# Kernel tuning notes

Measured on AMD Instinct MI355X. Metric: run time of the kernel, lower is better.

## Reference

```python
import jax, jax.numpy as jnp
import numpy as np

N_HEADS = 4


def setup_inputs() -> dict:
    key = jax.random.key(0)
    ks = jax.random.split(key, 6)
    B, T, N, D = 4, 16, 64, 256
    x = jax.random.normal(ks[0], (B, T, N, D), dtype=jnp.float32)
    bias_features = jax.random.normal(ks[1], (B, T, N, N, D), dtype=jnp.float32)
    mask = jax.random.randint(ks[2], (B, T, N), 0, 2).astype(bool)
    s = 1.0 / np.sqrt(D).astype(np.float32)
    Wqkv = jax.random.normal(ks[3], (D, 3 * D), dtype=jnp.float32) * s
    bqkv = jnp.zeros((3 * D,), dtype=jnp.float32)
    Wproj = jax.random.normal(ks[4], (D, D), dtype=jnp.float32) * s
    bproj = jnp.zeros((D,), dtype=jnp.float32)
    return {"x": x, "bias_features": bias_features, "mask": mask,
            "Wqkv": Wqkv, "bqkv": bqkv, "Wproj": Wproj, "bproj": bproj}


def reference(x, bias_features, mask, Wqkv, bqkv, Wproj, bproj):
    B, T, N, D = x.shape
    H = N_HEADS
    hd = D // H
    Batch = B * T
    scale = 1.0 / float(np.sqrt(hd))

    x_flat = x.reshape(Batch, N, D)
    qkv = x_flat @ Wqkv + bqkv                      # (Batch, N, 3D)
    q, k, v = jnp.split(qkv, 3, axis=-1)
    q = q.reshape(Batch, N, H, hd).transpose(0, 2, 1, 3)   # (Batch, H, N, hd)
    k = k.reshape(Batch, N, H, hd).transpose(0, 2, 1, 3)
    v = v.reshape(Batch, N, H, hd).transpose(0, 2, 1, 3)

    # geometry bias: (Batch, H, N, N, hd)
    b_geo = bias_features.reshape(Batch, N, N, H, hd).transpose(0, 3, 1, 2, 4)
    # per-pair dot of q[n] with geometry feature for pair (n, m)
    rel_scores = jnp.einsum("bhnd,bhnmd->bhnm", q, b_geo) * scale

    mask_flat = mask.reshape(Batch, 1, 1, N)
    attn_bias = jnp.where(mask_flat, rel_scores, jnp.float32(-1e9))

    scores = jnp.einsum("bhnd,bhmd->bhnm", q, k) * scale + attn_bias
    attn = jax.nn.softmax(scores, axis=-1)
    out = jnp.einsum("bhnm,bhmd->bhnd", attn, v)    # (Batch, H, N, hd)

    out = out.transpose(0, 2, 1, 3).reshape(Batch, N, D)
    out = out @ Wproj + bproj
    return out.reshape(B, T, N, D)
```

## Files before the change

kernel.cpp:

```cpp
#include <hip/hip_runtime.h>
#include <hip/hip_bf16.h>

#define BATCH 64
#define NRES 64
#define DMODEL 256
#define ROWS (BATCH*NRES)
#define QKVC 768
#define SCALE 0.125f
#define LDP 68

typedef float floatx4 __attribute__((ext_vector_type(4)));

__global__ __launch_bounds__(256) void qkv_gemm(
    const float* __restrict__ x, const float* __restrict__ W,
    const float* __restrict__ bq, float* __restrict__ qkv) {
  __shared__ float AsT[64 * LDP];
  __shared__ float Bs[64 * LDP];
  int t = threadIdx.x;
  int tx = t & 15, ty = t >> 4;
  int rowBase = blockIdx.y * 64;
  int colBase = blockIdx.x * 64;
  float acc[4][4] = {};
  for (int kb = 0; kb < 256; kb += 64) {
#pragma unroll
    for (int p = 0; p < 4; ++p) {
      int e = (p * 256 + t) * 4;
      int r = e >> 6, c = e & 63;
      float4 av = *(const float4*)&x[(size_t)(rowBase + r) * 256 + kb + c];
      AsT[(c + 0) * LDP + r] = av.x;
      AsT[(c + 1) * LDP + r] = av.y;
      AsT[(c + 2) * LDP + r] = av.z;
      AsT[(c + 3) * LDP + r] = av.w;
      *(float4*)&Bs[r * LDP + c] =
          *(const float4*)&W[(size_t)(kb + r) * QKVC + colBase + c];
    }
    __syncthreads();
#pragma unroll 4
    for (int kk = 0; kk < 64; ++kk) {
      float4 a4 = *(const float4*)&AsT[kk * LDP + ty * 4];
      float4 b4 = *(const float4*)&Bs[kk * LDP + tx * 4];
      float a[4] = {a4.x, a4.y, a4.z, a4.w};
      float b[4] = {b4.x, b4.y, b4.z, b4.w};
#pragma unroll
      for (int i = 0; i < 4; ++i)
#pragma unroll
        for (int j = 0; j < 4; ++j) acc[i][j] += a[i] * b[j];
    }
    __syncthreads();
  }
#pragma unroll
  for (int i = 0; i < 4; ++i) {
    int r = rowBase + ty * 4 + i;
#pragma unroll
    for (int j = 0; j < 4; ++j) {
      int c = colBase + tx * 4 + j;
      qkv[(size_t)r * QKVC + c] = acc[i][j] + bq[c];
    }
  }
}

__global__ __launch_bounds__(256) void qk_gemm(const float* __restrict__ qkv,
                                               float* __restrict__ qk) {
  __shared__ float qs[64 * 65];
  __shared__ float ks[64 * 65];
  int t = threadIdx.x;
  int bh = blockIdx.x;
  int b = bh >> 2, h = bh & 3;
  for (int i = 0; i < 16; ++i) {
    int idx = i * 256 + t;
    int r = idx >> 6, d = idx & 63;
    qs[r * 65 + d] = qkv[(size_t)(b * 64 + r) * QKVC + h * 64 + d];
    ks[r * 65 + d] = qkv[(size_t)(b * 64 + r) * QKVC + 256 + h * 64 + d];
  }
  __syncthreads();
  int m = t & 63, nq = t >> 6;
  for (int ni = 0; ni < 16; ++ni) {
    int n = nq * 16 + ni;
    float s = 0.f;
#pragma unroll 16
    for (int d = 0; d < 64; ++d) s += qs[n * 65 + d] * ks[m * 65 + d];
    qk[((size_t)bh * 64 + n) * 64 + m] = s;
  }
}

__global__ __launch_bounds__(256) void attn_kernel(
    const float* __restrict__ bias, const int* __restrict__ mask,
    const float* __restrict__ qkv, const float* __restrict__ qk,
    float* __restrict__ ctx) {
  __shared__ float q_s[256];
  __shared__ int mask_s[64];
  __shared__ float rel_s[256];
  __shared__ float attn_s[256];
  int t = threadIdx.x;
  int blk = blockIdx.x;
  int b = blk >> 6;
  int n_res = blk & 63;
  int m = t & 63, h = t >> 6;
  float s_qk = qk[(((size_t)(b * 4 + h) * 64 + n_res) * 64) + m];
  int msk = mask[b * 64 + m];
  if (t < 64) mask_s[t] = mask[b * 64 + t];
  q_s[t] = qkv[(size_t)blk * QKVC + t];
  __syncthreads();
  int wave = t >> 6, lane = t & 63;
  int hseg = lane >> 4;
  float4 qv = *(const float4*)&q_s[lane * 4];
  const floatx4* brow_base =
      (const floatx4*)(bias + (size_t)blk * 64 * 256);
#pragma unroll
  for (int i = 0; i < 16; ++i) {
    int mm = i * 4 + wave;
    if (mask_s[mm]) {
      floatx4 bv = __builtin_nontemporal_load(&brow_base[mm * 64 + lane]);
      float p = bv.x * qv.x + bv.y * qv.y + bv.z * qv.z + bv.w * qv.w;
      p += __shfl_xor(p, 1, 64);
      p += __shfl_xor(p, 2, 64);
      p += __shfl_xor(p, 4, 64);
      p += __shfl_xor(p, 8, 64);
      if ((lane & 15) == 0) rel_s[hseg * 64 + mm] = p;
    }
  }
  __syncthreads();
  float rel = rel_s[h * 64 + m];
  float logit = s_qk * SCALE + (msk ? rel * SCALE : -1e9f);
  float mx = logit;
#pragma unroll
  for (int off = 32; off > 0; off >>= 1) mx = fmaxf(mx, __shfl_xor(mx, off, 64));
  float ex = __expf(logit - mx);
  float sm = ex;
#pragma unroll
  for (int off = 32; off > 0; off >>= 1) sm += __shfl_xor(sm, off, 64);
  attn_s[h * 64 + m] = ex / sm;
  __syncthreads();
  int c = t;
  int hh = c >> 6;
  float acc = 0.f;
  const float* vbase = qkv + (size_t)b * 64 * QKVC + 512 + c;
#pragma unroll 8
  for (int mm = 0; mm < 64; ++mm) acc += attn_s[hh * 64 + mm] * vbase[(size_t)mm * QKVC];
  ctx[(size_t)blk * 256 + c] = acc;
}

__global__ __launch_bounds__(256) void proj_gemm(
    const float* __restrict__ ctx, const float* __restrict__ W,
    const float* __restrict__ bp, float* __restrict__ out) {
  __shared__ float AsT[64 * LDP];
  __shared__ float Bs[64 * LDP];
  int t = threadIdx.x;
  int tx = t & 15, ty = t >> 4;
  int rowBase = blockIdx.y * 64;
  int colBase = blockIdx.x * 64;
  float acc[4][4] = {};
  for (int kb = 0; kb < 256; kb += 64) {
#pragma unroll
    for (int p = 0; p < 4; ++p) {
      int e = (p * 256 + t) * 4;
      int r = e >> 6, c = e & 63;
      float4 av = *(const float4*)&ctx[(size_t)(rowBase + r) * 256 + kb + c];
      AsT[(c + 0) * LDP + r] = av.x;
      AsT[(c + 1) * LDP + r] = av.y;
      AsT[(c + 2) * LDP + r] = av.z;
      AsT[(c + 3) * LDP + r] = av.w;
      *(float4*)&Bs[r * LDP + c] =
          *(const float4*)&W[(size_t)(kb + r) * 256 + colBase + c];
    }
    __syncthreads();
#pragma unroll 4
    for (int kk = 0; kk < 64; ++kk) {
      float4 a4 = *(const float4*)&AsT[kk * LDP + ty * 4];
      float4 b4 = *(const float4*)&Bs[kk * LDP + tx * 4];
      float a[4] = {a4.x, a4.y, a4.z, a4.w};
      float b[4] = {b4.x, b4.y, b4.z, b4.w};
#pragma unroll
      for (int i = 0; i < 4; ++i)
#pragma unroll
        for (int j = 0; j < 4; ++j) acc[i][j] += a[i] * b[j];
    }
    __syncthreads();
  }
#pragma unroll
  for (int i = 0; i < 4; ++i) {
    int r = rowBase + ty * 4 + i;
#pragma unroll
    for (int j = 0; j < 4; ++j) {
      int c = colBase + tx * 4 + j;
      out[(size_t)r * 256 + c] = acc[i][j] + bp[c];
    }
  }
}

extern "C" void kernel_launch(void* const* d_in, const int* in_sizes, int n_in,
                              void* d_out, int out_size, void* d_ws, size_t ws_size,
                              hipStream_t stream) {
  const float* x    = (const float*)d_in[0];
  const float* bias = (const float*)d_in[1];
  const int*   mask = (const int*)d_in[2];
  const float* Wqkv = (const float*)d_in[3];
  const float* bqkv = (const float*)d_in[4];
  const float* Wprj = (const float*)d_in[5];
  const float* bprj = (const float*)d_in[6];
  float* out = (float*)d_out;

  float* qkv_ws = (float*)d_ws;
  float* qk_ws  = qkv_ws + (size_t)ROWS * QKVC;
  float* ctx_ws = qk_ws + (size_t)BATCH * 4 * 64 * 64;

  qkv_gemm<<<dim3(12, 64), 256, 0, stream>>>(x, Wqkv, bqkv, qkv_ws);
  qk_gemm<<<256, 256, 0, stream>>>(qkv_ws, qk_ws);
  attn_kernel<<<ROWS, 256, 0, stream>>>(bias, mask, qkv_ws, qk_ws, ctx_ws);
  proj_gemm<<<dim3(4, 64), 256, 0, stream>>>(ctx_ws, Wprj, bprj, out);
}
```

Before: 394.1 us.

## Fuse QK scores into attention kernel and vectorize PV with wave-split reduction

Removes the separate qk_gemm launch and its scratch buffer by computing q·k dot products inside the attention kernel, alongside the geometry-bias dot in the same shuffle-reduction loop. Masked bias rows are no longer skipped but redirected to row 0, so the loop has no branches. The PV product now uses float4 loads with each wave covering 16 keys, and a shared-memory reduction combines the four waves. Blocks are remapped so that groups of 8 consecutive block ids spread across batches. The trade-off is more shared memory and extra K reads per row in exchange for one less kernel launch and one less global round trip for the scores.

```diff
diff --git a/kernel.cpp b/kernel.cpp
--- a/kernel.cpp
+++ b/kernel.cpp
@@ -59,44 +59,20 @@
   }
 }
 
-__global__ __launch_bounds__(256) void qk_gemm(const float* __restrict__ qkv,
-                                               float* __restrict__ qk) {
-  __shared__ float qs[64 * 65];
-  __shared__ float ks[64 * 65];
-  int t = threadIdx.x;
-  int bh = blockIdx.x;
-  int b = bh >> 2, h = bh & 3;
-  for (int i = 0; i < 16; ++i) {
-    int idx = i * 256 + t;
-    int r = idx >> 6, d = idx & 63;
-    qs[r * 65 + d] = qkv[(size_t)(b * 64 + r) * QKVC + h * 64 + d];
-    ks[r * 65 + d] = qkv[(size_t)(b * 64 + r) * QKVC + 256 + h * 64 + d];
-  }
-  __syncthreads();
-  int m = t & 63, nq = t >> 6;
-  for (int ni = 0; ni < 16; ++ni) {
-    int n = nq * 16 + ni;
-    float s = 0.f;
-#pragma unroll 16
-    for (int d = 0; d < 64; ++d) s += qs[n * 65 + d] * ks[m * 65 + d];
-    qk[((size_t)bh * 64 + n) * 64 + m] = s;
-  }
-}
-
 __global__ __launch_bounds__(256) void attn_kernel(
     const float* __restrict__ bias, const int* __restrict__ mask,
-    const float* __restrict__ qkv, const float* __restrict__ qk,
-    float* __restrict__ ctx) {
+    const float* __restrict__ qkv, float* __restrict__ ctx) {
   __shared__ float q_s[256];
   __shared__ int mask_s[64];
   __shared__ float rel_s[256];
+  __shared__ float qks_s[256];
   __shared__ float attn_s[256];
+  __shared__ float red_s[4][256];
   int t = threadIdx.x;
-  int blk = blockIdx.x;
+  int logical = blockIdx.x;
+  int blk = (logical & 7) * 512 + (logical >> 3);
   int b = blk >> 6;
-  int n_res = blk & 63;
   int m = t & 63, h = t >> 6;
-  float s_qk = qk[(((size_t)(b * 4 + h) * 64 + n_res) * 64) + m];
   int msk = mask[b * 64 + m];
   if (t < 64) mask_s[t] = mask[b * 64 + t];
   q_s[t] = qkv[(size_t)blk * QKVC + t];
@@ -106,21 +82,32 @@
   float4 qv = *(const float4*)&q_s[lane * 4];
   const floatx4* brow_base =
       (const floatx4*)(bias + (size_t)blk * 64 * 256);
+  const floatx4* krow_base =
+      (const floatx4*)(qkv + (size_t)b * 64 * QKVC + 256);
 #pragma unroll
   for (int i = 0; i < 16; ++i) {
     int mm = i * 4 + wave;
-    if (mask_s[mm]) {
-      floatx4 bv = __builtin_nontemporal_load(&brow_base[mm * 64 + lane]);
-      float p = bv.x * qv.x + bv.y * qv.y + bv.z * qv.z + bv.w * qv.w;
-      p += __shfl_xor(p, 1, 64);
-      p += __shfl_xor(p, 2, 64);
-      p += __shfl_xor(p, 4, 64);
-      p += __shfl_xor(p, 8, 64);
-      if ((lane & 15) == 0) rel_s[hseg * 64 + mm] = p;
+    int src = mask_s[mm] ? mm : 0;
+    floatx4 bv = __builtin_nontemporal_load(&brow_base[src * 64 + lane]);
+    floatx4 kv = krow_base[(size_t)mm * (QKVC / 4) + lane];
+    float p = bv.x * qv.x + bv.y * qv.y + bv.z * qv.z + bv.w * qv.w;
+    float s = kv.x * qv.x + kv.y * qv.y + kv.z * qv.z + kv.w * qv.w;
+    p += __shfl_xor(p, 1, 64);
+    s += __shfl_xor(s, 1, 64);
+    p += __shfl_xor(p, 2, 64);
+    s += __shfl_xor(s, 2, 64);
+    p += __shfl_xor(p, 4, 64);
+    s += __shfl_xor(s, 4, 64);
+    p += __shfl_xor(p, 8, 64);
+    s += __shfl_xor(s, 8, 64);
+    if ((lane & 15) == 0) {
+      rel_s[hseg * 64 + mm] = p;
+      qks_s[hseg * 64 + mm] = s;
     }
   }
   __syncthreads();
   float rel = rel_s[h * 64 + m];
+  float s_qk = qks_s[h * 64 + m];
   float logit = s_qk * SCALE + (msk ? rel * SCALE : -1e9f);
   float mx = logit;
 #pragma unroll
@@ -131,13 +118,21 @@
   for (int off = 32; off > 0; off >>= 1) sm += __shfl_xor(sm, off, 64);
   attn_s[h * 64 + m] = ex / sm;
   __syncthreads();
-  int c = t;
-  int hh = c >> 6;
-  float acc = 0.f;
-  const float* vbase = qkv + (size_t)b * 64 * QKVC + 512 + c;
-#pragma unroll 8
-  for (int mm = 0; mm < 64; ++mm) acc += attn_s[hh * 64 + mm] * vbase[(size_t)mm * QKVC];
-  ctx[(size_t)blk * 256 + c] = acc;
+  int c4 = lane * 4;
+  int hh = lane >> 4;
+  floatx4 acc = {0.f, 0.f, 0.f, 0.f};
+  const float* vb = qkv + (size_t)b * 64 * QKVC + 512 + c4;
+#pragma unroll
+  for (int i = 0; i < 16; ++i) {
+    int mm = wave * 16 + i;
+    float a = attn_s[hh * 64 + mm];
+    floatx4 vv = *(const floatx4*)&vb[(size_t)mm * QKVC];
+    acc.x += a * vv.x; acc.y += a * vv.y; acc.z += a * vv.z; acc.w += a * vv.w;
+  }
+  *(floatx4*)&red_s[wave][c4] = acc;
+  __syncthreads();
+  ctx[(size_t)blk * 256 + t] =
+      red_s[0][t] + red_s[1][t] + red_s[2][t] + red_s[3][t];
 }
 
 __global__ __launch_bounds__(256) void proj_gemm(
@@ -201,11 +196,9 @@
   float* out = (float*)d_out;
 
   float* qkv_ws = (float*)d_ws;
-  float* qk_ws  = qkv_ws + (size_t)ROWS * QKVC;
-  float* ctx_ws = qk_ws + (size_t)BATCH * 4 * 64 * 64;
+  float* ctx_ws = qkv_ws + (size_t)ROWS * QKVC;
 
   qkv_gemm<<<dim3(12, 64), 256, 0, stream>>>(x, Wqkv, bqkv, qkv_ws);
-  qk_gemm<<<256, 256, 0, stream>>>(qkv_ws, qk_ws);
-  attn_kernel<<<ROWS, 256, 0, stream>>>(bias, mask, qkv_ws, qk_ws, ctx_ws);
+  attn_kernel<<<ROWS, 256, 0, stream>>>(bias, mask, qkv_ws, ctx_ws);
   proj_gemm<<<dim3(4, 64), 256, 0, stream>>>(ctx_ws, Wprj, bprj, out);
 }
```

New measurement: 397.4 us. No clear change (+0.8%).
